# Optimization experiments

Measured on AMD Instinct MI355X. Metric: run time of the kernel, lower is better.

The kernel has to match this reference:

```python
import jax, jax.numpy as jnp
import numpy as np

D_MODEL = 64
TEMPER = float(np.power(D_MODEL, 0.5))  # d_model ** temper_value
B, L, DK = 64, 1024, 64
P = 2 * L - 1  # relative position range


def setup_inputs() -> dict:
    key = jax.random.key(0)
    k1, k2, k3, k4, k5 = jax.random.split(key, 5)
    q = jax.random.normal(k1, (B, L, DK), dtype=jnp.float32)
    k = jax.random.normal(k2, (B, L, DK), dtype=jnp.float32)
    v = jax.random.normal(k3, (B, L, DK), dtype=jnp.float32)
    position_dpa = jax.random.normal(k4, (B, P, DK), dtype=jnp.float32)
    attn_mask = jax.random.uniform(k5, (B, L, L)) < 0.1
    return {"q": q, "k": k, "v": v, "position_dpa": position_dpa, "attn_mask": attn_mask}


def reference(q, k, v, position_dpa, attn_mask):
    # q,k,v: [B, L, d]; position_dpa: [B, 2L-1, d]; attn_mask: [B, L, L] bool
    Lq = q.shape[1]
    attn = jnp.einsum('bld,bmd->blm', q, k) / TEMPER            # [B, L, L]
    attn_pos = jnp.einsum('bld,bpd->blp', q, position_dpa) / TEMPER  # [B, L, 2L-1]
    # Replicates batch_stripe(flip(attn_pos.transpose(1,2), -1)).transpose(1,2):
    # bias[b, i, j] = attn_pos[b, L-1-i, i+j]
    i = jnp.arange(Lq)
    rows = (Lq - 1) - i[:, None]                 # [L, 1]
    cols = i[:, None] + i[None, :]               # [L, L], values in [0, 2L-2]
    bias = attn_pos[:, rows, cols]               # [B, L, L]
    attn = attn + bias
    attn = jnp.where(attn_mask, -jnp.inf, attn)
    attn = jax.nn.softmax(attn, axis=-1)
    # dropout is identity in eval mode
    output = jnp.einsum('blm,bmd->bld', attn, v)  # [B, L, d]
    return output, attn
```

## Files before the change

### kernel.cpp

```cpp
#include <hip/hip_runtime.h>

#define BN   64
#define LN   1024
#define DKN  64
#define PN   2047
#define OUT_O_ELEMS ((size_t)BN * LN * DKN)
constexpr float kScale = 0.125f;

typedef short bf16x8 __attribute__((ext_vector_type(8)));
typedef float f32x4  __attribute__((ext_vector_type(4)));

__device__ __forceinline__ unsigned short f2b(float f) {
  return (unsigned short)((__float_as_uint(f) + 0x8000u) >> 16);
}
__device__ __forceinline__ float b2f(unsigned short h) {
  return __uint_as_float(((unsigned)h) << 16);
}
__device__ __forceinline__ unsigned pk2(float x, float y) {
  unsigned lo = (__float_as_uint(x) + 0x8000u) >> 16;
  unsigned hi = (__float_as_uint(y) + 0x8000u) & 0xFFFF0000u;
  return lo | hi;
}

union U8 { unsigned u[4]; bf16x8 v; };

__device__ __forceinline__ bf16x8 pack8(float4 a, float4 b) {
  U8 r;
  r.u[0] = pk2(a.x, a.y); r.u[1] = pk2(a.z, a.w);
  r.u[2] = pk2(b.x, b.y); r.u[3] = pk2(b.z, b.w);
  return r.v;
}

__global__ void flag_init(unsigned* f) { *f = 0u; }

__global__ void flag_scan(const unsigned* __restrict__ mw, unsigned* f) {
  int idx = blockIdx.x * 256 + threadIdx.x;
  unsigned bits = 0;
#pragma unroll
  for (int i = 0; i < 4; ++i) {
    unsigned wv = mw[idx * 4 + i];
    if (wv == 0x3F800000u) bits |= 2u;
    else if (wv > 1u)      bits |= 4u;
  }
  if (bits) atomicOr(f, bits);
}

__global__ __launch_bounds__(256) void convert2_f32_bf16(const float4* __restrict__ a,
                                                         uint2* __restrict__ oa, int na,
                                                         const float4* __restrict__ bsrc,
                                                         uint2* __restrict__ ob) {
  int idx = blockIdx.x * 256 + threadIdx.x;
  if (idx < na) {
    float4 x = a[idx];
    oa[idx] = make_uint2(pk2(x.x, x.y), pk2(x.z, x.w));
  } else {
    int j = idx - na;
    float4 x = bsrc[j];
    ob[j] = make_uint2(pk2(x.x, x.y), pk2(x.z, x.w));
  }
}

__global__ __launch_bounds__(256) void transpose_v(const float4* __restrict__ vg,
                                                   short* __restrict__ vt) {
  __shared__ float tile[64 * 65];
  const int tid = threadIdx.x;
  const int b  = blockIdx.x >> 4;
  const int mt = blockIdx.x & 15;
  const size_t base = ((size_t)b * 1024 + mt * 64) * 16;
#pragma unroll
  for (int i = 0; i < 4; ++i) {
    int j = tid + (i << 8);
    float4 a = vg[base + j];
    float* d = &tile[(j >> 4) * 65 + ((j & 15) << 2)];
    d[0] = a.x; d[1] = a.y; d[2] = a.z; d[3] = a.w;
  }
  __syncthreads();
#pragma unroll
  for (int i = 0; i < 4; ++i) {
    int j  = tid + (i << 8);
    int d  = j >> 4;
    int mq = (j & 15) << 2;
    unsigned u0 = pk2(tile[(mq + 0) * 65 + d], tile[(mq + 1) * 65 + d]);
    unsigned u1 = pk2(tile[(mq + 2) * 65 + d], tile[(mq + 3) * 65 + d]);
    size_t idx = ((size_t)b * 64 + d) * 1024 + mt * 64 + mq;
    *(uint2*)(vt + idx) = make_uint2(u0, u1);
  }
}

__global__ __launch_bounds__(256, 8)
void attn_kernel(const float* __restrict__ qf, const float* __restrict__ kf,
                 const float* __restrict__ vf, const float* __restrict__ pf,
                 const void* __restrict__ mask, const unsigned* __restrict__ flagp,
                 const short* __restrict__ k16, const short* __restrict__ p16,
                 const short* __restrict__ vt16,
                 float* __restrict__ out) {
  __shared__ short E[16 * 1024];

  const int tid  = threadIdx.x;
  const int w    = tid >> 6;
  const int lane = tid & 63;
  const int col  = lane & 15;
  const int quad = lane >> 4;

  int p   = blockIdx.x;
  int xcd = p & 7;
  int qq  = p >> 3;
  int rt  = qq & 63;
  int bh  = qq >> 6;
  const int b  = (bh << 3) | xcd;
  const int l0 = rt << 4;

  unsigned mflag = flagp ? flagp[0] : 0u;
  const int mkind = (mflag & 4u) ? 1 : ((mflag & 2u) ? 2 : 0);

  const float4* qg = (const float4*)qf;
  const size_t qrow  = ((size_t)b * LN + (size_t)(l0 + col)) * 16 + (size_t)(quad * 2);
  const size_t qrrow = ((size_t)b * LN + (size_t)(LN - 1 - l0 - col)) * 16 + (size_t)(quad * 2);
  const bf16x8 aq0 = pack8(qg[qrow],      qg[qrow + 1]);
  const bf16x8 aq1 = pack8(qg[qrow + 8],  qg[qrow + 9]);
  const bf16x8 ar0 = pack8(qg[qrrow],     qg[qrrow + 1]);
  const bf16x8 ar1 = pack8(qg[qrrow + 8], qg[qrrow + 9]);

  const int moff = (w << 4) + col;
  const size_t mrow0 = (((size_t)b << 10) + (size_t)(l0 + (quad << 2))) << 10;

  if (k16) {
    struct KPM { bf16x8 k0, k1, p00, p01, p10, p11; unsigned m[4]; };
    KPM A, Bf;

    auto LOAD = [&](int t, KPM& o) {
      const int m0 = t << 6, mglob = m0 + moff;
      const short* kr = k16 + ((size_t)b * LN + mglob) * DKN + quad * 8;
      o.k0 = *(const bf16x8*)kr;
      o.k1 = *(const bf16x8*)(kr + 32);
      int g0 = l0 + m0 + moff;
      int g1 = g0 + 16; if (g1 > PN - 1) g1 = PN - 1;
      const short* pr0 = p16 + ((size_t)b * PN + g0) * DKN + quad * 8;
      const short* pr1 = p16 + ((size_t)b * PN + g1) * DKN + quad * 8;
      o.p00 = *(const bf16x8*)pr0;
      o.p01 = *(const bf16x8*)(pr0 + 32);
      o.p10 = *(const bf16x8*)pr1;
      o.p11 = *(const bf16x8*)(pr1 + 32);
      const size_t mi = mrow0 + (size_t)mglob;
      if (mkind == 1) {
        const unsigned char* mp = (const unsigned char*)mask + mi;
#pragma unroll
        for (int r = 0; r < 4; ++r) o.m[r] = __builtin_nontemporal_load(mp + ((size_t)r << 10));
      } else {
        const unsigned* mp = (const unsigned*)mask + mi;
#pragma unroll
        for (int r = 0; r < 4; ++r) o.m[r] = __builtin_nontemporal_load(mp + ((size_t)r << 10));
      }
    };

    auto COMP = [&](int t, KPM& o) {
      f32x4 qk = {0.f, 0.f, 0.f, 0.f};
      qk = __builtin_amdgcn_mfma_f32_16x16x32_bf16(aq0, o.k0, qk, 0, 0, 0);
      qk = __builtin_amdgcn_mfma_f32_16x16x32_bf16(aq1, o.k1, qk, 0, 0, 0);
      f32x4 ba = {0.f, 0.f, 0.f, 0.f}, bb = {0.f, 0.f, 0.f, 0.f};
      ba = __builtin_amdgcn_mfma_f32_16x16x32_bf16(ar0, o.p00, ba, 0, 0, 0);
      ba = __builtin_amdgcn_mfma_f32_16x16x32_bf16(ar1, o.p01, ba, 0, 0, 0);
      bb = __builtin_amdgcn_mfma_f32_16x16x32_bf16(ar0, o.p10, bb, 0, 0, 0);
      bb = __builtin_amdgcn_mfma_f32_16x16x32_bf16(ar1, o.p11, bb, 0, 0, 0);
      const int mglob = (t << 6) + moff;
#pragma unroll
      for (int r = 0; r < 4; ++r) {
        int i = (quad << 2) + r;
        int o2 = i + col;
        int srcLane = (lane & 48) | (o2 & 15);
        float va = __shfl(ba[r], srcLane);
        float vb = __shfl(bb[r], srcLane);
        float bias = (o2 < 16) ? va : vb;
        float s = (qk[r] + bias) * kScale;
        float e = o.m[r] ? 0.f : __expf(s);
        E[i * 1024 + (mglob ^ ((i & 7) << 3))] = (short)f2b(e);
      }
    };

    LOAD(0, A);
    for (int t = 0; t < 16; t += 2) {
      LOAD(t + 1, Bf);
      COMP(t, A);
      if (t < 14) LOAD(t + 2, A);
      COMP(t + 1, Bf);
    }
  } else {
    for (int t = 0; t < 16; ++t) {
      const int m0 = t << 6, mglob = m0 + moff;
      int g0 = l0 + m0 + moff;
      int g1 = g0 + 16; if (g1 > PN - 1) g1 = PN - 1;
      const float4* kr = (const float4*)(kf + ((size_t)b * LN + mglob) * DKN);
      bf16x8 kb0 = pack8(kr[quad * 2], kr[quad * 2 + 1]);
      bf16x8 kb1 = pack8(kr[8 + quad * 2], kr[9 + quad * 2]);
      const float4* pr0 = (const float4*)(pf + ((size_t)b * PN + g0) * DKN);
      const float4* pr1 = (const float4*)(pf + ((size_t)b * PN + g1) * DKN);
      bf16x8 pb00 = pack8(pr0[quad * 2], pr0[quad * 2 + 1]);
      bf16x8 pb01 = pack8(pr0[8 + quad * 2], pr0[9 + quad * 2]);
      bf16x8 pb10 = pack8(pr1[quad * 2], pr1[quad * 2 + 1]);
      bf16x8 pb11 = pack8(pr1[8 + quad * 2], pr1[9 + quad * 2]);

      f32x4 qk = {0.f, 0.f, 0.f, 0.f};
      qk = __builtin_amdgcn_mfma_f32_16x16x32_bf16(aq0, kb0, qk, 0, 0, 0);
      qk = __builtin_amdgcn_mfma_f32_16x16x32_bf16(aq1, kb1, qk, 0, 0, 0);
      f32x4 ba = {0.f, 0.f, 0.f, 0.f}, bb = {0.f, 0.f, 0.f, 0.f};
      ba = __builtin_amdgcn_mfma_f32_16x16x32_bf16(ar0, pb00, ba, 0, 0, 0);
      ba = __builtin_amdgcn_mfma_f32_16x16x32_bf16(ar1, pb01, ba, 0, 0, 0);
      bb = __builtin_amdgcn_mfma_f32_16x16x32_bf16(ar0, pb10, bb, 0, 0, 0);
      bb = __builtin_amdgcn_mfma_f32_16x16x32_bf16(ar1, pb11, bb, 0, 0, 0);

#pragma unroll
      for (int r = 0; r < 4; ++r) {
        int i = (quad << 2) + r;
        int o2 = i + col;
        int srcLane = (lane & 48) | (o2 & 15);
        float va = __shfl(ba[r], srcLane);
        float vb = __shfl(bb[r], srcLane);
        float bias = (o2 < 16) ? va : vb;
        float s = (qk[r] + bias) * kScale;
        size_t mi = mrow0 + ((size_t)r << 10) + (size_t)mglob;
        unsigned mu = (mkind == 1) ? (unsigned)((const unsigned char*)mask)[mi]
                                   : ((const unsigned*)mask)[mi];
        float e = mu ? 0.f : __expf(s);
        E[i * 1024 + (mglob ^ ((i & 7) << 3))] = (short)f2b(e);
      }
    }
  }
  __syncthreads();

  f32x4 acc = {0.f, 0.f, 0.f, 0.f};
  float sLo = 0.f, sHi = 0.f;
  const int drow = moff;
  const int esw  = (col & 7) << 3;

  auto EAT = [&](bf16x8 ev) {
    U8 u; u.v = ev;
#pragma unroll
    for (int j = 0; j < 4; ++j) {
      sLo += __uint_as_float(u.u[j] << 16);
      sHi += __uint_as_float(u.u[j] & 0xFFFF0000u);
    }
  };

  if (vt16) {
    const short* vbase = vt16 + ((size_t)b * 64 + drow) * 1024 + quad * 8;
    bf16x8 v0A = *(const bf16x8*)vbase;
    bf16x8 v1A = *(const bf16x8*)(vbase + 32);
    bf16x8 v0B, v1B;
    for (int t = 0; t < 16; t += 2) {
      { const short* vr = vbase + ((t + 1) << 6);
        v0B = *(const bf16x8*)vr; v1B = *(const bf16x8*)(vr + 32); }
      { const int m0 = t << 6;
        bf16x8 ea0 = *(const bf16x8*)&E[col * 1024 + ((m0 + quad * 8) ^ esw)];
        bf16x8 ea1 = *(const bf16x8*)&E[col * 1024 + ((m0 + 32 + quad * 8) ^ esw)];
        acc = __builtin_amdgcn_mfma_f32_16x16x32_bf16(ea0, v0A, acc, 0, 0, 0);
        acc = __builtin_amdgcn_mfma_f32_16x16x32_bf16(ea1, v1A, acc, 0, 0, 0);
        EAT(ea0); EAT(ea1); }
      if (t < 14) { const short* vr = vbase + ((t + 2) << 6);
        v0A = *(const bf16x8*)vr; v1A = *(const bf16x8*)(vr + 32); }
      { const int m0 = (t + 1) << 6;
        bf16x8 ea0 = *(const bf16x8*)&E[col * 1024 + ((m0 + quad * 8) ^ esw)];
        bf16x8 ea1 = *(const bf16x8*)&E[col * 1024 + ((m0 + 32 + quad * 8) ^ esw)];
        acc = __builtin_amdgcn_mfma_f32_16x16x32_bf16(ea0, v0B, acc, 0, 0, 0);
        acc = __builtin_amdgcn_mfma_f32_16x16x32_bf16(ea1, v1B, acc, 0, 0, 0);
        EAT(ea0); EAT(ea1); }
    }
  } else {
    for (int t = 0; t < 16; ++t) {
      const int m0 = t << 6;
      const float* vc = vf + ((size_t)b * LN + m0) * DKN + drow;
      U8 t0, t1;
#pragma unroll
      for (int j = 0; j < 4; ++j) {
        t0.u[j] = pk2(vc[(quad * 8 + 2 * j) * 64],      vc[(quad * 8 + 2 * j + 1) * 64]);
        t1.u[j] = pk2(vc[(32 + quad * 8 + 2 * j) * 64], vc[(32 + quad * 8 + 2 * j + 1) * 64]);
      }
      bf16x8 ea0 = *(const bf16x8*)&E[col * 1024 + ((m0 + quad * 8) ^ esw)];
      bf16x8 ea1 = *(const bf16x8*)&E[col * 1024 + ((m0 + 32 + quad * 8) ^ esw)];
      acc = __builtin_amdgcn_mfma_f32_16x16x32_bf16(ea0, t0.v, acc, 0, 0, 0);
      acc = __builtin_amdgcn_mfma_f32_16x16x32_bf16(ea1, t1.v, acc, 0, 0, 0);
      EAT(ea0); EAT(ea1);
    }
  }

  float s = sLo + sHi;
  s += __shfl_xor(s, 16);
  s += __shfl_xor(s, 32);
  const float invS = 1.0f / s;

#pragma unroll
  for (int r = 0; r < 4; ++r) {
    int i = (quad << 2) + r;
    float invi = __shfl(invS, (lane & 48) | i);
    out[(((size_t)b << 10) + (size_t)(l0 + i)) * 64 + drow] = acc[r] * invi;
  }

  float* outA = out + OUT_O_ELEMS;
  const size_t aBase = (((size_t)b << 10) + (size_t)l0) << 10;
  for (int t = 0; t < 16; ++t) {
    float inv = __shfl(invS, (lane & 48) | t);
    const ushort4 ev = *(const ushort4*)&E[t * 1024 + ((tid << 2) ^ ((t & 7) << 3))];
    f32x4 o4;
    o4[0] = b2f(ev.x) * inv;
    o4[1] = b2f(ev.y) * inv;
    o4[2] = b2f(ev.z) * inv;
    o4[3] = b2f(ev.w) * inv;
    __builtin_nontemporal_store(o4, (f32x4*)&outA[aBase + ((size_t)t << 10) + (size_t)(tid << 2)]);
  }
}

extern "C" void kernel_launch(void* const* d_in, const int* in_sizes, int n_in,
                              void* d_out, int out_size, void* d_ws, size_t ws_size,
                              hipStream_t stream) {
  const float* q   = (const float*)d_in[0];
  const float* k   = (const float*)d_in[1];
  const float* v   = (const float*)d_in[2];
  const float* pos = (const float*)d_in[3];
  const void* mask = d_in[4];
  float* out = (float*)d_out;

  unsigned* flag = nullptr;
  if (ws_size >= 256) {
    flag = (unsigned*)d_ws;
    flag_init<<<1, 1, 0, stream>>>(flag);
    flag_scan<<<64, 256, 0, stream>>>((const unsigned*)mask, flag);
  }

  const size_t kElems  = (size_t)BN * LN * DKN;
  const size_t pElems  = (size_t)BN * PN * DKN;
  const size_t offK    = 256;
  const size_t offP    = offK + kElems * 2;
  const size_t offVT   = offP + pElems * 2;
  const size_t wsNeed  = offVT + kElems * 2;

  short *k16 = nullptr, *p16 = nullptr, *vt16 = nullptr;
  if (ws_size >= wsNeed) {
    char* base = (char*)d_ws;
    k16  = (short*)(base + offK);
    p16  = (short*)(base + offP);
    vt16 = (short*)(base + offVT);
    const int na = (int)(kElems / 4);
    const int nb = (int)(pElems / 4);
    convert2_f32_bf16<<<(na + nb) / 256, 256, 0, stream>>>((const float4*)k, (uint2*)k16, na,
                                                           (const float4*)pos, (uint2*)p16);
    transpose_v<<<BN * 16, 256, 0, stream>>>((const float4*)v, vt16);
  }

  attn_kernel<<<BN * (LN / 16), 256, 0, stream>>>(q, k, v, pos, mask, flag,
                                                  k16, p16, vt16, out);
}
```

Baseline: 698.0 us.

## Pre-pack mask to bitmask and compute row sums via MFMA with ones

Adds a pack_mask pre-pass that compresses the boolean mask into 16-bit column bitmasks per 16-row tile, so the attention kernel reads one short per column instead of four byte/word loads. Row sums of the softmax numerator are now computed with extra MFMAs against a ones vector instead of scalar bf16 unpacking and shuffles. Launch bounds occupancy hint is lowered from 8 to 5. The extra pass still reads the full mask once and adds a launch plus workspace, and doubles MFMA count in the PV loop.

```diff
diff --git a/kernel.cpp b/kernel.cpp
--- a/kernel.cpp
+++ b/kernel.cpp
@@ -43,6 +43,39 @@
     else if (wv > 1u)      bits |= 4u;
   }
   if (bits) atomicOr(f, bits);
+}
+
+__global__ __launch_bounds__(256) void pack_mask(const void* __restrict__ mask,
+                                                 const unsigned* __restrict__ flagp,
+                                                 unsigned short* __restrict__ mb) {
+  const int t  = threadIdx.x;
+  const size_t rowBase = (size_t)blockIdx.x << 4;
+  unsigned mflag = flagp ? flagp[0] : 0u;
+  const int mkind = (mflag & 4u) ? 1 : ((mflag & 2u) ? 2 : 0);
+  unsigned b0 = 0, b1 = 0, b2 = 0, b3 = 0;
+  if (mkind == 1) {
+    const unsigned* mp = (const unsigned*)mask;
+#pragma unroll
+    for (int i = 0; i < 16; ++i) {
+      unsigned wv = mp[((rowBase + i) << 8) + t];
+      if (wv & 0x000000FFu) b0 |= (1u << i);
+      if (wv & 0x0000FF00u) b1 |= (1u << i);
+      if (wv & 0x00FF0000u) b2 |= (1u << i);
+      if (wv & 0xFF000000u) b3 |= (1u << i);
+    }
+  } else {
+    const uint4* mp = (const uint4*)mask;
+#pragma unroll
+    for (int i = 0; i < 16; ++i) {
+      uint4 wv = mp[((rowBase + i) << 8) + t];
+      if (wv.x) b0 |= (1u << i);
+      if (wv.y) b1 |= (1u << i);
+      if (wv.z) b2 |= (1u << i);
+      if (wv.w) b3 |= (1u << i);
+    }
+  }
+  *(uint2*)(mb + ((size_t)blockIdx.x << 10) + (t << 2)) =
+      make_uint2(b0 | (b1 << 16), b2 | (b3 << 16));
 }
 
 __global__ __launch_bounds__(256) void convert2_f32_bf16(const float4* __restrict__ a,
@@ -87,12 +120,12 @@
   }
 }
 
-__global__ __launch_bounds__(256, 8)
+__global__ __launch_bounds__(256, 5)
 void attn_kernel(const float* __restrict__ qf, const float* __restrict__ kf,
                  const float* __restrict__ vf, const float* __restrict__ pf,
                  const void* __restrict__ mask, const unsigned* __restrict__ flagp,
                  const short* __restrict__ k16, const short* __restrict__ p16,
-                 const short* __restrict__ vt16,
+                 const short* __restrict__ vt16, const unsigned short* __restrict__ maskBp,
                  float* __restrict__ out) {
   __shared__ short E[16 * 1024];
 
@@ -123,6 +156,7 @@
 
   const int moff = (w << 4) + col;
   const size_t mrow0 = (((size_t)b << 10) + (size_t)(l0 + (quad << 2))) << 10;
+  const unsigned short* mbRow = maskBp ? (maskBp + (((size_t)(b << 6) + rt) << 10)) : nullptr;
 
   if (k16) {
     struct KPM { bf16x8 k0, k1, p00, p01, p10, p11; unsigned m[4]; };
@@ -141,15 +175,19 @@
       o.p01 = *(const bf16x8*)(pr0 + 32);
       o.p10 = *(const bf16x8*)pr1;
       o.p11 = *(const bf16x8*)(pr1 + 32);
-      const size_t mi = mrow0 + (size_t)mglob;
-      if (mkind == 1) {
-        const unsigned char* mp = (const unsigned char*)mask + mi;
-#pragma unroll
-        for (int r = 0; r < 4; ++r) o.m[r] = __builtin_nontemporal_load(mp + ((size_t)r << 10));
+      if (mbRow) {
+        o.m[0] = mbRow[mglob];
       } else {
-        const unsigned* mp = (const unsigned*)mask + mi;
-#pragma unroll
-        for (int r = 0; r < 4; ++r) o.m[r] = __builtin_nontemporal_load(mp + ((size_t)r << 10));
+        const size_t mi = mrow0 + (size_t)mglob;
+        if (mkind == 1) {
+          const unsigned char* mp = (const unsigned char*)mask + mi;
+#pragma unroll
+          for (int r = 0; r < 4; ++r) o.m[r] = __builtin_nontemporal_load(mp + ((size_t)r << 10));
+        } else {
+          const unsigned* mp = (const unsigned*)mask + mi;
+#pragma unroll
+          for (int r = 0; r < 4; ++r) o.m[r] = __builtin_nontemporal_load(mp + ((size_t)r << 10));
+        }
       }
     };
 
@@ -172,7 +210,8 @@
         float vb = __shfl(bb[r], srcLane);
         float bias = (o2 < 16) ? va : vb;
         float s = (qk[r] + bias) * kScale;
-        float e = o.m[r] ? 0.f : __expf(s);
+        bool msk = mbRow ? (((o.m[0] >> i) & 1u) != 0u) : (o.m[r] != 0u);
+        float e = msk ? 0.f : __expf(s);
         E[i * 1024 + (mglob ^ ((i & 7) << 3))] = (short)f2b(e);
       }
     };
@@ -227,19 +266,12 @@
   }
   __syncthreads();
 
-  f32x4 acc = {0.f, 0.f, 0.f, 0.f};
-  float sLo = 0.f, sHi = 0.f;
+  f32x4 acc  = {0.f, 0.f, 0.f, 0.f};
+  f32x4 acc2 = {0.f, 0.f, 0.f, 0.f};
+  U8 onesU; onesU.u[0] = onesU.u[1] = onesU.u[2] = onesU.u[3] = 0x3F803F80u;
+  const bf16x8 ONE = onesU.v;
   const int drow = moff;
   const int esw  = (col & 7) << 3;
-
-  auto EAT = [&](bf16x8 ev) {
-    U8 u; u.v = ev;
-#pragma unroll
-    for (int j = 0; j < 4; ++j) {
-      sLo += __uint_as_float(u.u[j] << 16);
-      sHi += __uint_as_float(u.u[j] & 0xFFFF0000u);
-    }
-  };
 
   if (vt16) {
     const short* vbase = vt16 + ((size_t)b * 64 + drow) * 1024 + quad * 8;
@@ -252,17 +284,19 @@
       { const int m0 = t << 6;
         bf16x8 ea0 = *(const bf16x8*)&E[col * 1024 + ((m0 + quad * 8) ^ esw)];
         bf16x8 ea1 = *(const bf16x8*)&E[col * 1024 + ((m0 + 32 + quad * 8) ^ esw)];
-        acc = __builtin_amdgcn_mfma_f32_16x16x32_bf16(ea0, v0A, acc, 0, 0, 0);
-        acc = __builtin_amdgcn_mfma_f32_16x16x32_bf16(ea1, v1A, acc, 0, 0, 0);
-        EAT(ea0); EAT(ea1); }
+        acc  = __builtin_amdgcn_mfma_f32_16x16x32_bf16(ea0, v0A, acc,  0, 0, 0);
+        acc  = __builtin_amdgcn_mfma_f32_16x16x32_bf16(ea1, v1A, acc,  0, 0, 0);
+        acc2 = __builtin_amdgcn_mfma_f32_16x16x32_bf16(ea0, ONE, acc2, 0, 0, 0);
+        acc2 = __builtin_amdgcn_mfma_f32_16x16x32_bf16(ea1, ONE, acc2, 0, 0, 0); }
       if (t < 14) { const short* vr = vbase + ((t + 2) << 6);
         v0A = *(const bf16x8*)vr; v1A = *(const bf16x8*)(vr + 32); }
       { const int m0 = (t + 1) << 6;
         bf16x8 ea0 = *(const bf16x8*)&E[col * 1024 + ((m0 + quad * 8) ^ esw)];
         bf16x8 ea1 = *(const bf16x8*)&E[col * 1024 + ((m0 + 32 + quad * 8) ^ esw)];
-        acc = __builtin_amdgcn_mfma_f32_16x16x32_bf16(ea0, v0B, acc, 0, 0, 0);
-        acc = __builtin_amdgcn_mfma_f32_16x16x32_bf16(ea1, v1B, acc, 0, 0, 0);
-        EAT(ea0); EAT(ea1); }
+        acc  = __builtin_amdgcn_mfma_f32_16x16x32_bf16(ea0, v0B, acc,  0, 0, 0);
+        acc  = __builtin_amdgcn_mfma_f32_16x16x32_bf16(ea1, v1B, acc,  0, 0, 0);
+        acc2 = __builtin_amdgcn_mfma_f32_16x16x32_bf16(ea0, ONE, acc2, 0, 0, 0);
+        acc2 = __builtin_amdgcn_mfma_f32_16x16x32_bf16(ea1, ONE, acc2, 0, 0, 0); }
     }
   } else {
     for (int t = 0; t < 16; ++t) {
@@ -276,28 +310,28 @@
       }
       bf16x8 ea0 = *(const bf16x8*)&E[col * 1024 + ((m0 + quad * 8) ^ esw)];
       bf16x8 ea1 = *(const bf16x8*)&E[col * 1024 + ((m0 + 32 + quad * 8) ^ esw)];
-      acc = __builtin_amdgcn_mfma_f32_16x16x32_bf16(ea0, t0.v, acc, 0, 0, 0);
-      acc = __builtin_amdgcn_mfma_f32_16x16x32_bf16(ea1, t1.v, acc, 0, 0, 0);
-      EAT(ea0); EAT(ea1);
-    }
-  }
-
-  float s = sLo + sHi;
-  s += __shfl_xor(s, 16);
-  s += __shfl_xor(s, 32);
-  const float invS = 1.0f / s;
+      acc  = __builtin_amdgcn_mfma_f32_16x16x32_bf16(ea0, t0.v, acc,  0, 0, 0);
+      acc  = __builtin_amdgcn_mfma_f32_16x16x32_bf16(ea1, t1.v, acc,  0, 0, 0);
+      acc2 = __builtin_amdgcn_mfma_f32_16x16x32_bf16(ea0, ONE, acc2, 0, 0, 0);
+      acc2 = __builtin_amdgcn_mfma_f32_16x16x32_bf16(ea1, ONE, acc2, 0, 0, 0);
+    }
+  }
+
+  float invR[4];
+#pragma unroll
+  for (int r = 0; r < 4; ++r) invR[r] = 1.0f / acc2[r];
 
 #pragma unroll
   for (int r = 0; r < 4; ++r) {
     int i = (quad << 2) + r;
-    float invi = __shfl(invS, (lane & 48) | i);
-    out[(((size_t)b << 10) + (size_t)(l0 + i)) * 64 + drow] = acc[r] * invi;
+    out[(((size_t)b << 10) + (size_t)(l0 + i)) * 64 + drow] = acc[r] * invR[r];
   }
 
   float* outA = out + OUT_O_ELEMS;
   const size_t aBase = (((size_t)b << 10) + (size_t)l0) << 10;
+#pragma unroll
   for (int t = 0; t < 16; ++t) {
-    float inv = __shfl(invS, (lane & 48) | t);
+    float inv = __shfl(invR[t & 3], (t >> 2) << 4);
     const ushort4 ev = *(const ushort4*)&E[t * 1024 + ((tid << 2) ^ ((t & 7) << 3))];
     f32x4 o4;
     o4[0] = b2f(ev.x) * inv;
@@ -330,9 +364,13 @@
   const size_t offK    = 256;
   const size_t offP    = offK + kElems * 2;
   const size_t offVT   = offP + pElems * 2;
-  const size_t wsNeed  = offVT + kElems * 2;
+  const size_t offMB   = offVT + kElems * 2;
+  const size_t mbBytes = (size_t)BN * 64 * 1024 * 2;
+  const size_t wsNeed  = offMB;
+  const size_t wsFull  = offMB + mbBytes;
 
   short *k16 = nullptr, *p16 = nullptr, *vt16 = nullptr;
+  unsigned short* maskB = nullptr;
   if (ws_size >= wsNeed) {
     char* base = (char*)d_ws;
     k16  = (short*)(base + offK);
@@ -343,8 +381,12 @@
     convert2_f32_bf16<<<(na + nb) / 256, 256, 0, stream>>>((const float4*)k, (uint2*)k16, na,
                                                            (const float4*)pos, (uint2*)p16);
     transpose_v<<<BN * 16, 256, 0, stream>>>((const float4*)v, vt16);
+    if (ws_size >= wsFull && flag) {
+      maskB = (unsigned short*)(base + offMB);
+      pack_mask<<<BN * 64, 256, 0, stream>>>(mask, flag, maskB);
+    }
   }
 
   attn_kernel<<<BN * (LN / 16), 256, 0, stream>>>(q, k, v, pos, mask, flag,
-                                                  k16, p16, vt16, out);
-}
+                                                  k16, p16, vt16, maskB, out);
+}
```

New measurement: 885.5 us. 26.9% more time.
